# Optimization experiments

Measured on AMD Instinct MI355X. Metric: run time of the kernel, lower is better.

Reference implementation:

```python
import jax, jax.numpy as jnp
import numpy as np

B, C, H, W = 8, 256, 64, 64
RED = 16

def setup_inputs() -> dict:
    key = jax.random.key(0)
    ks = jax.random.split(key, 10)
    s = 0.05
    return {
        "x": jax.random.normal(ks[0], (B, C, H, W), jnp.float32),
        "ca_w1": jax.random.normal(ks[1], (C // RED, C), jnp.float32) * s,
        "ca_w2": jax.random.normal(ks[2], (C, C // RED), jnp.float32) * s,
        "q_w": jax.random.normal(ks[3], (C // RED, C), jnp.float32) * s,
        "q_b": jax.random.normal(ks[4], (C // RED,), jnp.float32) * s,
        "k_w": jax.random.normal(ks[5], (C // RED, C), jnp.float32) * s,
        "k_b": jax.random.normal(ks[6], (C // RED,), jnp.float32) * s,
        "v_w": jax.random.normal(ks[7], (C, C), jnp.float32) * s,
        "v_b": jax.random.normal(ks[8], (C,), jnp.float32) * s,
        "gamma": jax.random.normal(ks[9], (1,), jnp.float32) * s,
    }

def _cbam(x, ca_w1, ca_w2, q_w, q_b, k_w, k_b, v_w, v_b, gamma):
    # ---- Channel attention (squeeze-excite with avg+max pooling) ----
    avg = jnp.mean(x, axis=(2, 3))          # [B, C]
    mx = jnp.max(x, axis=(2, 3))            # [B, C]
    def fc(s):
        h = jax.nn.relu(jnp.einsum('rc,bc->br', ca_w1, s))
        return jnp.einsum('cr,br->bc', ca_w2, h)
    gate = jax.nn.sigmoid(fc(avg) + fc(mx))[:, :, None, None]
    x = x * gate
    # ---- Spatial (non-local) attention ----
    b, c, h, w = x.shape
    hw = h * w
    xf = x.reshape(b, c, hw)                          # [B, C, HW]
    q = jnp.einsum('rc,bcn->brn', q_w, xf) + q_b[None, :, None]   # [B, C/r, HW]
    k = jnp.einsum('rc,bcn->brn', k_w, xf) + k_b[None, :, None]
    v = jnp.einsum('oc,bcn->bon', v_w, xf) + v_b[None, :, None]   # [B, C, HW]
    attn = jax.nn.softmax(jnp.einsum('bri,brj->bij', q, k), axis=-1)  # [B, HW, HW]
    out = jnp.einsum('bcj,bij->bci', v, attn).reshape(b, c, h, w)
    return gamma[0] * out + x

def reference(x, ca_w1, ca_w2, q_w, q_b, k_w, k_b, v_w, v_b, gamma):
    return _cbam(x, ca_w1, ca_w2, q_w, q_b, k_w, k_b, v_w, v_b, gamma)
```

## Files before the change

kernel.cpp:

```cpp
#include <hip/hip_runtime.h>
#include <hip/hip_bf16.h>
#include <math.h>

#define BB 8
#define CCH 256
#define HWN 4096
#define RR 16
#define PSTR 72

typedef __attribute__((ext_vector_type(8))) short short8;
typedef __attribute__((ext_vector_type(4))) float f32x4;

static __device__ __forceinline__ unsigned short f2bf(float x) {
    union { float f; unsigned u; } v; v.f = x;
    return (unsigned short)((v.u + 0x8000u) >> 16);
}
static __device__ __forceinline__ unsigned bfr(float x) {
    union { float f; unsigned u; } v; v.f = x;
    return v.u + 0x8000u;
}

__global__ __launch_bounds__(256) void k_pool(const float* __restrict__ x,
                                              float* __restrict__ avgp,
                                              float* __restrict__ maxp) {
    int bc = blockIdx.x;
    const float4* p = (const float4*)(x + (size_t)bc * HWN);
    int t = threadIdx.x;
    float s = 0.f, m = -INFINITY;
#pragma unroll
    for (int i = 0; i < 4; ++i) {
        float4 v = p[t + 256 * i];
        s += v.x + v.y + v.z + v.w;
        m = fmaxf(m, fmaxf(fmaxf(v.x, v.y), fmaxf(v.z, v.w)));
    }
    for (int off = 32; off; off >>= 1) {
        s += __shfl_down(s, off);
        m = fmaxf(m, __shfl_down(m, off));
    }
    __shared__ float ss[4], sm[4];
    int wid = t >> 6;
    if ((t & 63) == 0) { ss[wid] = s; sm[wid] = m; }
    __syncthreads();
    if (t == 0) {
        float S = ss[0] + ss[1] + ss[2] + ss[3];
        float M = fmaxf(fmaxf(sm[0], sm[1]), fmaxf(sm[2], sm[3]));
        avgp[bc] = S * (1.f / (float)HWN);
        maxp[bc] = M;
    }
}

__global__ __launch_bounds__(256) void k_gate(const float* __restrict__ avgp,
                                              const float* __restrict__ maxp,
                                              const float* __restrict__ w1,
                                              const float* __restrict__ w2,
                                              float* __restrict__ gate) {
    int b = blockIdx.x, t = threadIdx.x;
    __shared__ float sa[CCH], sx[CCH], sh[32];
    sa[t] = avgp[b * CCH + t];
    sx[t] = maxp[b * CCH + t];
    __syncthreads();
    if (t < 32) {
        int r = t & 15;
        const float* src = (t < 16) ? sa : sx;
        float h = 0.f;
        for (int c = 0; c < CCH; ++c) h += w1[r * CCH + c] * src[c];
        sh[t] = fmaxf(h, 0.f);
    }
    __syncthreads();
    float g = 0.f;
#pragma unroll
    for (int r = 0; r < RR; ++r) g += w2[t * RR + r] * (sh[r] + sh[16 + r]);
    gate[b * CCH + t] = 1.f / (1.f + __expf(-g));
}

__global__ __launch_bounds__(256) void k_wprep(const float* __restrict__ vw,
                                               const float* __restrict__ qw,
                                               const float* __restrict__ kw,
                                               unsigned short* __restrict__ Wb) {
    int idx = blockIdx.x * 256 + threadIdx.x;
    int m = idx >> 8, c = idx & 255;
    float v;
    if (m < 256) v = vw[idx];
    else if (m < 272) v = qw[(m - 256) * 256 + c];
    else v = kw[(m - 272) * 256 + c];
    Wb[idx] = f2bf(v);
}

__global__ __launch_bounds__(256) void k_proj(const float* __restrict__ x,
                                              const float* __restrict__ gate,
                                              const unsigned short* __restrict__ Wb,
                                              const float* __restrict__ vb,
                                              const float* __restrict__ qb,
                                              const float* __restrict__ kb,
                                              unsigned short* __restrict__ qT,
                                              unsigned short* __restrict__ kT,
                                              unsigned short* __restrict__ vB) {
    int b = blockIdx.x & 7;
    int n0 = (blockIdx.x >> 3) << 6;
    int t = threadIdx.x;
    int w = t >> 6, l = t & 63, quad = l >> 4, ln = l & 15;

    __shared__ __align__(16) unsigned short xs_t[64][72];
    __shared__ __align__(16) unsigned short vtile[256 * 72];
    __shared__ float qk_s[32][66];

    const f32x4 zf = {0.f, 0.f, 0.f, 0.f};
    f32x4 acc[18];
#pragma unroll
    for (int mt = 0; mt < 18; ++mt) acc[mt] = zf;

    for (int cc = 0; cc < 4; ++cc) {
        __syncthreads();
#pragma unroll
        for (int it = 0; it < 4; ++it) {
            int idx = it * 256 + t;
            int cl = idx >> 4, nq = idx & 15;
            int c = cc * 64 + cl;
            float g = gate[b * CCH + c];
            float4 v = *(const float4*)(x + (((size_t)(b * CCH + c)) << 12) + n0 + nq * 4);
            xs_t[nq * 4 + 0][cl] = f2bf(v.x * g);
            xs_t[nq * 4 + 1][cl] = f2bf(v.y * g);
            xs_t[nq * 4 + 2][cl] = f2bf(v.z * g);
            xs_t[nq * 4 + 3][cl] = f2bf(v.w * g);
        }
        __syncthreads();

        short8 bfrag[2];
#pragma unroll
        for (int kc = 0; kc < 2; ++kc)
            bfrag[kc] = *(const short8*)&xs_t[w * 16 + ln][kc * 32 + quad * 8];

#pragma unroll
        for (int mt = 0; mt < 18; ++mt) {
#pragma unroll
            for (int kc = 0; kc < 2; ++kc) {
                short8 af = *(const short8*)(Wb + ((size_t)(mt * 16 + ln)) * 256 + cc * 64 + kc * 32 + quad * 8);
                acc[mt] = __builtin_amdgcn_mfma_f32_16x16x32_bf16(af, bfrag[kc], acc[mt], 0, 0, 0);
            }
        }
    }

#pragma unroll
    for (int mt = 0; mt < 16; ++mt) {
#pragma unroll
        for (int r = 0; r < 4; ++r) {
            int m = mt * 16 + quad * 4 + r;
            vtile[m * 72 + w * 16 + ln] = f2bf(acc[mt][r] + vb[m]);
        }
    }
#pragma unroll
    for (int r = 0; r < 4; ++r) {
        qk_s[quad * 4 + r][w * 16 + ln] = acc[16][r];
        qk_s[16 + quad * 4 + r][w * 16 + ln] = acc[17][r];
    }
    __syncthreads();

    {
        unsigned short* vBp = vB + (((size_t)b) << 20);
        int c = t;
#pragma unroll
        for (int Q = 0; Q < 8; ++Q) {
            short8 v8 = *(const short8*)(vtile + c * 72 + Q * 8);
            *(short8*)(vBp + ((size_t)((((n0 >> 3) + Q) << 8) + c) << 3)) = v8;
        }
    }
    if (t < 128) {
        int isK = t >> 6;
        int n = t & 63;
        const float* bias = isK ? kb : qb;
        unsigned u32[8];
#pragma unroll
        for (int j = 0; j < 8; ++j) {
            unsigned lo = f2bf(qk_s[isK * 16 + 2 * j][n] + bias[2 * j]);
            unsigned hi = f2bf(qk_s[isK * 16 + 2 * j + 1][n] + bias[2 * j + 1]);
            u32[j] = lo | (hi << 16);
        }
        unsigned short* dst = (isK ? kT : qT) + ((size_t)(b * HWN + n0 + n)) * RR;
        uint4 d0 = {u32[0], u32[1], u32[2], u32[3]};
        uint4 d1 = {u32[4], u32[5], u32[6], u32[7]};
        ((uint4*)dst)[0] = d0;
        ((uint4*)dst)[1] = d1;
    }
}

__global__ __launch_bounds__(512, 4) void k_attn(const unsigned short* __restrict__ qT,
                                                 const unsigned short* __restrict__ kT,
                                                 const unsigned short* __restrict__ vB,
                                                 const float* __restrict__ x,
                                                 const float* __restrict__ gate,
                                                 const float* __restrict__ gamma,
                                                 float* __restrict__ out) {
    int b = blockIdx.x & 7;
    int i0 = (blockIdx.x >> 3) << 5;
    int t = threadIdx.x;
    int w = t >> 6, l = t & 63;
    int quad = l >> 4, ln = l & 15;
    int isub = w & 1, jsub = w >> 1;
    int c0 = w * 32;

    __shared__ __align__(16) unsigned short p_lds[2][32 * PSTR];
    __shared__ float l_s[4][36];

    const short8 zs = {0, 0, 0, 0, 0, 0, 0, 0};
    const f32x4 zf = {0.f, 0.f, 0.f, 0.f};

    short8 bq = zs;
    if (quad < 2)
        bq = *(const short8*)(qT + (((size_t)(b * HWN + i0 + isub * 16 + ln)) << 4) + (quad << 3));

    f32x4 acc[2][2];
#pragma unroll
    for (int cs = 0; cs < 2; ++cs)
#pragma unroll
        for (int is = 0; is < 2; ++is) acc[cs][is] = zf;
    float lsum = 0.f;

    const float c1 = 1.44269504f;
    const float c0e = -11.5415603f;

    const unsigned short* vbase = vB + (((size_t)b) << 20) + ((size_t)c0 << 3);
    const unsigned short* kbase = kT + ((size_t)(b * HWN)) * RR;

    short8 akA = zs, akB = zs;
    short8 avA[4], avB[4];

    auto load_ak = [&](short8& ak, int j0) {
        if (quad < 2)
            ak = *(const short8*)(kbase + (((size_t)(j0 + jsub * 16 + ln)) << 4) + (quad << 3));
    };
    auto load_av = [&](short8 (&av)[4], int j0) {
#pragma unroll
        for (int ks = 0; ks < 2; ++ks)
#pragma unroll
            for (int cs = 0; cs < 2; ++cs) {
                int jc = (j0 >> 3) + ks * 4 + quad;
                av[ks * 2 + cs] = *(const short8*)(vbase + ((size_t)(((jc << 8) + cs * 16 + ln)) << 3));
            }
    };

    load_ak(akA, 0);
    load_av(avA, 0);

    auto step = [&](short8& akC, short8 (&avC)[4], short8& akN, short8 (&avN)[4],
                    unsigned short* pbuf, int j0n, bool pf) {
        f32x4 sf = __builtin_amdgcn_mfma_f32_16x16x32_bf16(akC, bq, zf, 0, 0, 0);

        float p0 = exp2f(fmaf(sf[0], c1, c0e));
        float p1 = exp2f(fmaf(sf[1], c1, c0e));
        float p2 = exp2f(fmaf(sf[2], c1, c0e));
        float p3 = exp2f(fmaf(sf[3], c1, c0e));
        lsum += (p0 + p1) + (p2 + p3);
        uint2 pk;
        pk.x = (bfr(p0) >> 16) | (bfr(p1) & 0xFFFF0000u);
        pk.y = (bfr(p2) >> 16) | (bfr(p3) & 0xFFFF0000u);
        *(uint2*)(pbuf + (isub * 16 + ln) * PSTR + jsub * 16 + quad * 4) = pk;

        __syncthreads();

        if (pf) { load_ak(akN, j0n); load_av(avN, j0n); }

#pragma unroll
        for (int ks = 0; ks < 2; ++ks) {
            short8 bp[2];
#pragma unroll
            for (int is = 0; is < 2; ++is)
                bp[is] = *(const short8*)(pbuf + (is * 16 + ln) * PSTR + ks * 32 + quad * 8);
#pragma unroll
            for (int cs = 0; cs < 2; ++cs)
#pragma unroll
                for (int is = 0; is < 2; ++is)
                    acc[cs][is] = __builtin_amdgcn_mfma_f32_16x16x32_bf16(avC[ks * 2 + cs], bp[is], acc[cs][is], 0, 0, 0);
        }
    };

    for (int jt2 = 0; jt2 < 32; ++jt2) {
        int j0 = jt2 << 7;
        step(akA, avA, akB, avB, &p_lds[0][0], j0 + 64, true);
        step(akB, avB, akA, avA, &p_lds[1][0], (jt2 < 31) ? (j0 + 128) : 0, jt2 < 31);
    }

    lsum += __shfl_xor(lsum, 16, 64);
    lsum += __shfl_xor(lsum, 32, 64);
    if (l < 16) l_s[jsub][isub * 16 + l] = lsum;
    __syncthreads();

    float g = gamma[0];
    float rinv[2];
#pragma unroll
    for (int is = 0; is < 2; ++is) {
        int i = is * 16 + ln;
        float lf = (l_s[0][i] + l_s[1][i]) + (l_s[2][i] + l_s[3][i]);
        rinv[is] = g / lf;
    }

#pragma unroll
    for (int cs = 0; cs < 2; ++cs) {
#pragma unroll
        for (int r = 0; r < 4; ++r) {
            int c = c0 + cs * 16 + quad * 4 + r;
            float gc = gate[b * CCH + c];
            size_t rowoff = (((size_t)(b * CCH + c)) << 12) + i0;
            float* po = out + rowoff;
            const float* px = x + rowoff;
#pragma unroll
            for (int is = 0; is < 2; ++is) {
                int idx = is * 16 + ln;
                po[idx] = acc[cs][is][r] * rinv[is] + px[idx] * gc;
            }
        }
    }
}

extern "C" void kernel_launch(void* const* d_in, const int* in_sizes, int n_in,
                              void* d_out, int out_size, void* d_ws, size_t ws_size,
                              hipStream_t stream) {
    const float* x = (const float*)d_in[0];
    const float* w1 = (const float*)d_in[1];
    const float* w2 = (const float*)d_in[2];
    const float* qw = (const float*)d_in[3];
    const float* qb = (const float*)d_in[4];
    const float* kw = (const float*)d_in[5];
    const float* kb = (const float*)d_in[6];
    const float* vw = (const float*)d_in[7];
    const float* vb = (const float*)d_in[8];
    const float* gamma = (const float*)d_in[9];
    float* out = (float*)d_out;
    char* ws = (char*)d_ws;

    float* avgp = (float*)(ws);
    float* maxp = (float*)(ws + 8192);
    float* gate = (float*)(ws + 16384);
    unsigned short* Wb = (unsigned short*)(ws + 24576);
    unsigned short* qT = (unsigned short*)(ws + 24576 + 147456);
    unsigned short* kT = (unsigned short*)(ws + 24576 + 147456 + 1048576);
    unsigned short* vB = (unsigned short*)(ws + 24576 + 147456 + 2097152);

    k_pool<<<2048, 256, 0, stream>>>(x, avgp, maxp);
    k_wprep<<<288, 256, 0, stream>>>(vw, qw, kw, Wb);
    k_gate<<<8, 256, 0, stream>>>(avgp, maxp, w1, w2, gate);
    k_proj<<<512, 256, 0, stream>>>(x, gate, Wb, vb, qb, kb, qT, kT, vB);
    k_attn<<<1024, 512, 0, stream>>>(qT, kT, vB, x, gate, gamma, out);
}
```

Measured before the change: 257.7 us.

## Restructure attention kernel to 16-query tiles with 4 waves and swizzled LDS

The attention kernel now handles 16 query rows per block with 256 threads (4 waves), launching 2048 blocks instead of 1024. Each wave owns 64 output channels and one 16-key slice of the score tile. The padded P buffer is replaced by an XOR-swizzled 16x64 LDS layout to avoid bank conflicts. The V loads are now issued after the PV MMAs into a single register set rather than double-buffered. Total V and K reads from memory double because each block covers half as many queries. The intent is more resident blocks and fewer registers per thread, but the V prefetch now sits right behind its use, which may expose load latency.

```diff
diff --git a/kernel.cpp b/kernel.cpp
--- a/kernel.cpp
+++ b/kernel.cpp
@@ -6,7 +6,6 @@
 #define CCH 256
 #define HWN 4096
 #define RR 16
-#define PSTR 72
 
 typedef __attribute__((ext_vector_type(8))) short short8;
 typedef __attribute__((ext_vector_type(4))) float f32x4;
@@ -183,7 +182,7 @@
     }
 }
 
-__global__ __launch_bounds__(512, 4) void k_attn(const unsigned short* __restrict__ qT,
+__global__ __launch_bounds__(256, 6) void k_attn(const unsigned short* __restrict__ qT,
                                                  const unsigned short* __restrict__ kT,
                                                  const unsigned short* __restrict__ vB,
                                                  const float* __restrict__ x,
@@ -191,28 +190,25 @@
                                                  const float* __restrict__ gamma,
                                                  float* __restrict__ out) {
     int b = blockIdx.x & 7;
-    int i0 = (blockIdx.x >> 3) << 5;
+    int i0 = (blockIdx.x >> 3) << 4;
     int t = threadIdx.x;
     int w = t >> 6, l = t & 63;
     int quad = l >> 4, ln = l & 15;
-    int isub = w & 1, jsub = w >> 1;
-    int c0 = w * 32;
-
-    __shared__ __align__(16) unsigned short p_lds[2][32 * PSTR];
-    __shared__ float l_s[4][36];
+    int c0 = w * 64;
+
+    __shared__ __align__(16) unsigned short p_lds[2][16 * 64];
+    __shared__ float l_s[4][20];
 
     const short8 zs = {0, 0, 0, 0, 0, 0, 0, 0};
     const f32x4 zf = {0.f, 0.f, 0.f, 0.f};
 
     short8 bq = zs;
     if (quad < 2)
-        bq = *(const short8*)(qT + (((size_t)(b * HWN + i0 + isub * 16 + ln)) << 4) + (quad << 3));
-
-    f32x4 acc[2][2];
-#pragma unroll
-    for (int cs = 0; cs < 2; ++cs)
-#pragma unroll
-        for (int is = 0; is < 2; ++is) acc[cs][is] = zf;
+        bq = *(const short8*)(qT + (((size_t)(b * HWN + i0 + ln)) << 4) + (quad << 3));
+
+    f32x4 acc[4];
+#pragma unroll
+    for (int cs = 0; cs < 4; ++cs) acc[cs] = zf;
     float lsum = 0.f;
 
     const float c1 = 1.44269504f;
@@ -221,30 +217,29 @@
     const unsigned short* vbase = vB + (((size_t)b) << 20) + ((size_t)c0 << 3);
     const unsigned short* kbase = kT + ((size_t)(b * HWN)) * RR;
 
+    int key = ln & 7;
+    int soff = ln * 64 + (((w * 2 + (quad >> 1)) ^ key) * 2 + (quad & 1)) * 4;
+    int roff0 = ln * 64 + ((quad ^ key) << 3);
+    int roff1 = ln * 64 + (((4 + quad) ^ key) << 3);
+
     short8 akA = zs, akB = zs;
-    short8 avA[4], avB[4];
+    short8 av[8];
 
     auto load_ak = [&](short8& ak, int j0) {
         if (quad < 2)
-            ak = *(const short8*)(kbase + (((size_t)(j0 + jsub * 16 + ln)) << 4) + (quad << 3));
+            ak = *(const short8*)(kbase + (((size_t)(j0 + w * 16 + ln)) << 4) + (quad << 3));
     };
-    auto load_av = [&](short8 (&av)[4], int j0) {
+    auto load_av = [&](int j0) {
 #pragma unroll
         for (int ks = 0; ks < 2; ++ks)
 #pragma unroll
-            for (int cs = 0; cs < 2; ++cs) {
+            for (int cs = 0; cs < 4; ++cs) {
                 int jc = (j0 >> 3) + ks * 4 + quad;
-                av[ks * 2 + cs] = *(const short8*)(vbase + ((size_t)(((jc << 8) + cs * 16 + ln)) << 3));
+                av[ks * 4 + cs] = *(const short8*)(vbase + ((size_t)(((jc << 8) + cs * 16 + ln)) << 3));
             }
     };
-
-    load_ak(akA, 0);
-    load_av(avA, 0);
-
-    auto step = [&](short8& akC, short8 (&avC)[4], short8& akN, short8 (&avN)[4],
-                    unsigned short* pbuf, int j0n, bool pf) {
+    auto sstep = [&](short8& akC, unsigned short* pbuf) {
         f32x4 sf = __builtin_amdgcn_mfma_f32_16x16x32_bf16(akC, bq, zf, 0, 0, 0);
-
         float p0 = exp2f(fmaf(sf[0], c1, c0e));
         float p1 = exp2f(fmaf(sf[1], c1, c0e));
         float p2 = exp2f(fmaf(sf[2], c1, c0e));
@@ -253,60 +248,55 @@
         uint2 pk;
         pk.x = (bfr(p0) >> 16) | (bfr(p1) & 0xFFFF0000u);
         pk.y = (bfr(p2) >> 16) | (bfr(p3) & 0xFFFF0000u);
-        *(uint2*)(pbuf + (isub * 16 + ln) * PSTR + jsub * 16 + quad * 4) = pk;
-
-        __syncthreads();
-
-        if (pf) { load_ak(akN, j0n); load_av(avN, j0n); }
-
-#pragma unroll
-        for (int ks = 0; ks < 2; ++ks) {
-            short8 bp[2];
-#pragma unroll
-            for (int is = 0; is < 2; ++is)
-                bp[is] = *(const short8*)(pbuf + (is * 16 + ln) * PSTR + ks * 32 + quad * 8);
-#pragma unroll
-            for (int cs = 0; cs < 2; ++cs)
-#pragma unroll
-                for (int is = 0; is < 2; ++is)
-                    acc[cs][is] = __builtin_amdgcn_mfma_f32_16x16x32_bf16(avC[ks * 2 + cs], bp[is], acc[cs][is], 0, 0, 0);
-        }
+        *(uint2*)(pbuf + soff) = pk;
     };
+    auto pvstep = [&](const unsigned short* pbuf) {
+        short8 bp0 = *(const short8*)(pbuf + roff0);
+#pragma unroll
+        for (int cs = 0; cs < 4; ++cs)
+            acc[cs] = __builtin_amdgcn_mfma_f32_16x16x32_bf16(av[cs], bp0, acc[cs], 0, 0, 0);
+        short8 bp1 = *(const short8*)(pbuf + roff1);
+#pragma unroll
+        for (int cs = 0; cs < 4; ++cs)
+            acc[cs] = __builtin_amdgcn_mfma_f32_16x16x32_bf16(av[4 + cs], bp1, acc[cs], 0, 0, 0);
+    };
+
+    load_ak(akA, 0);
+    load_av(0);
 
     for (int jt2 = 0; jt2 < 32; ++jt2) {
         int j0 = jt2 << 7;
-        step(akA, avA, akB, avB, &p_lds[0][0], j0 + 64, true);
-        step(akB, avB, akA, avA, &p_lds[1][0], (jt2 < 31) ? (j0 + 128) : 0, jt2 < 31);
+        sstep(akA, &p_lds[0][0]);
+        __syncthreads();
+        load_ak(akB, j0 + 64);
+        pvstep(&p_lds[0][0]);
+        load_av(j0 + 64);
+
+        int j0n = (jt2 < 31) ? (j0 + 128) : 0;
+        sstep(akB, &p_lds[1][0]);
+        __syncthreads();
+        load_ak(akA, j0n);
+        pvstep(&p_lds[1][0]);
+        load_av(j0n);
     }
 
     lsum += __shfl_xor(lsum, 16, 64);
     lsum += __shfl_xor(lsum, 32, 64);
-    if (l < 16) l_s[jsub][isub * 16 + l] = lsum;
+    if (l < 16) l_s[w][l] = lsum;
     __syncthreads();
 
     float g = gamma[0];
-    float rinv[2];
-#pragma unroll
-    for (int is = 0; is < 2; ++is) {
-        int i = is * 16 + ln;
-        float lf = (l_s[0][i] + l_s[1][i]) + (l_s[2][i] + l_s[3][i]);
-        rinv[is] = g / lf;
-    }
-
-#pragma unroll
-    for (int cs = 0; cs < 2; ++cs) {
+    float lf = (l_s[0][ln] + l_s[1][ln]) + (l_s[2][ln] + l_s[3][ln]);
+    float rinv = g / lf;
+
+#pragma unroll
+    for (int cs = 0; cs < 4; ++cs) {
 #pragma unroll
         for (int r = 0; r < 4; ++r) {
             int c = c0 + cs * 16 + quad * 4 + r;
             float gc = gate[b * CCH + c];
             size_t rowoff = (((size_t)(b * CCH + c)) << 12) + i0;
-            float* po = out + rowoff;
-            const float* px = x + rowoff;
-#pragma unroll
-            for (int is = 0; is < 2; ++is) {
-                int idx = is * 16 + ln;
-                po[idx] = acc[cs][is][r] * rinv[is] + px[idx] * gc;
-            }
+            out[rowoff + ln] = acc[cs][r] * rinv + x[rowoff + ln] * gc;
         }
     }
 }
@@ -339,5 +329,5 @@
     k_wprep<<<288, 256, 0, stream>>>(vw, qw, kw, Wb);
     k_gate<<<8, 256, 0, stream>>>(avgp, maxp, w1, w2, gate);
     k_proj<<<512, 256, 0, stream>>>(x, gate, Wb, vb, qb, kb, qT, kT, vB);
-    k_attn<<<1024, 512, 0, stream>>>(qT, kT, vB, x, gate, gamma, out);
-}
+    k_attn<<<2048, 256, 0, stream>>>(qT, kT, vB, x, gate, gamma, out);
+}
```

Result: slower. 557.3 us (+116.2%).

## Double attention query tile to 64 rows to halve V streaming per block

Applied to the files above, without the earlier changes.

Each attention block now covers 64 query positions instead of 32, with the 8 waves split 4 along i and 2 along j. Every V and K tile loaded is therefore reused for twice as many query rows, roughly halving V and K traffic across the grid, and each wave issues more MFMAs per softmax tile. The V prefetch is now single-buffered and issued after the PV MFMAs, and the LDS row stride changes from 72 to 68. The cost is fewer blocks (512), more accumulator registers, and less load-latency hiding for V.

```diff
diff --git a/kernel.cpp b/kernel.cpp
--- a/kernel.cpp
+++ b/kernel.cpp
@@ -6,7 +6,7 @@
 #define CCH 256
 #define HWN 4096
 #define RR 16
-#define PSTR 72
+#define PSTR 68
 
 typedef __attribute__((ext_vector_type(8))) short short8;
 typedef __attribute__((ext_vector_type(4))) float f32x4;
@@ -191,28 +191,28 @@
                                                  const float* __restrict__ gamma,
                                                  float* __restrict__ out) {
     int b = blockIdx.x & 7;
-    int i0 = (blockIdx.x >> 3) << 5;
+    int i0 = (blockIdx.x >> 3) << 6;
     int t = threadIdx.x;
     int w = t >> 6, l = t & 63;
     int quad = l >> 4, ln = l & 15;
-    int isub = w & 1, jsub = w >> 1;
+    int iw = w & 3, jw = w >> 2;
     int c0 = w * 32;
 
-    __shared__ __align__(16) unsigned short p_lds[2][32 * PSTR];
-    __shared__ float l_s[4][36];
+    __shared__ __align__(16) unsigned short p_lds[2][64 * PSTR];
+    __shared__ float l_s[8][20];
 
     const short8 zs = {0, 0, 0, 0, 0, 0, 0, 0};
     const f32x4 zf = {0.f, 0.f, 0.f, 0.f};
 
     short8 bq = zs;
     if (quad < 2)
-        bq = *(const short8*)(qT + (((size_t)(b * HWN + i0 + isub * 16 + ln)) << 4) + (quad << 3));
-
-    f32x4 acc[2][2];
+        bq = *(const short8*)(qT + (((size_t)(b * HWN + i0 + iw * 16 + ln)) << 4) + (quad << 3));
+
+    f32x4 acc[2][4];
 #pragma unroll
     for (int cs = 0; cs < 2; ++cs)
 #pragma unroll
-        for (int is = 0; is < 2; ++is) acc[cs][is] = zf;
+        for (int is = 0; is < 4; ++is) acc[cs][is] = zf;
     float lsum = 0.f;
 
     const float c1 = 1.44269504f;
@@ -221,14 +221,22 @@
     const unsigned short* vbase = vB + (((size_t)b) << 20) + ((size_t)c0 << 3);
     const unsigned short* kbase = kT + ((size_t)(b * HWN)) * RR;
 
-    short8 akA = zs, akB = zs;
-    short8 avA[4], avB[4];
-
-    auto load_ak = [&](short8& ak, int j0) {
-        if (quad < 2)
-            ak = *(const short8*)(kbase + (((size_t)(j0 + jsub * 16 + ln)) << 4) + (quad << 3));
+    int soff0 = (iw * 16 + ln) * PSTR + jw * 32 + quad * 4;
+    int soff1 = soff0 + 16;
+
+    short8 akA[2], akB[2];
+    short8 av[4];
+#pragma unroll
+    for (int jt = 0; jt < 2; ++jt) { akA[jt] = zs; akB[jt] = zs; }
+
+    auto load_ak = [&](short8 (&ak)[2], int j0) {
+        if (quad < 2) {
+#pragma unroll
+            for (int jt = 0; jt < 2; ++jt)
+                ak[jt] = *(const short8*)(kbase + (((size_t)(j0 + jw * 32 + jt * 16 + ln)) << 4) + (quad << 3));
+        }
     };
-    auto load_av = [&](short8 (&av)[4], int j0) {
+    auto load_av = [&](int j0) {
 #pragma unroll
         for (int ks = 0; ks < 2; ++ks)
 #pragma unroll
@@ -237,61 +245,71 @@
                 av[ks * 2 + cs] = *(const short8*)(vbase + ((size_t)(((jc << 8) + cs * 16 + ln)) << 3));
             }
     };
-
-    load_ak(akA, 0);
-    load_av(avA, 0);
-
-    auto step = [&](short8& akC, short8 (&avC)[4], short8& akN, short8 (&avN)[4],
-                    unsigned short* pbuf, int j0n, bool pf) {
-        f32x4 sf = __builtin_amdgcn_mfma_f32_16x16x32_bf16(akC, bq, zf, 0, 0, 0);
-
-        float p0 = exp2f(fmaf(sf[0], c1, c0e));
-        float p1 = exp2f(fmaf(sf[1], c1, c0e));
-        float p2 = exp2f(fmaf(sf[2], c1, c0e));
-        float p3 = exp2f(fmaf(sf[3], c1, c0e));
-        lsum += (p0 + p1) + (p2 + p3);
+    auto sstep = [&](short8 (&akC)[2], unsigned short* pbuf) {
+        f32x4 sf0 = __builtin_amdgcn_mfma_f32_16x16x32_bf16(akC[0], bq, zf, 0, 0, 0);
+        f32x4 sf1 = __builtin_amdgcn_mfma_f32_16x16x32_bf16(akC[1], bq, zf, 0, 0, 0);
+        float p0 = exp2f(fmaf(sf0[0], c1, c0e));
+        float p1 = exp2f(fmaf(sf0[1], c1, c0e));
+        float p2 = exp2f(fmaf(sf0[2], c1, c0e));
+        float p3 = exp2f(fmaf(sf0[3], c1, c0e));
+        float q0 = exp2f(fmaf(sf1[0], c1, c0e));
+        float q1 = exp2f(fmaf(sf1[1], c1, c0e));
+        float q2 = exp2f(fmaf(sf1[2], c1, c0e));
+        float q3 = exp2f(fmaf(sf1[3], c1, c0e));
+        lsum += ((p0 + p1) + (p2 + p3)) + ((q0 + q1) + (q2 + q3));
         uint2 pk;
         pk.x = (bfr(p0) >> 16) | (bfr(p1) & 0xFFFF0000u);
         pk.y = (bfr(p2) >> 16) | (bfr(p3) & 0xFFFF0000u);
-        *(uint2*)(pbuf + (isub * 16 + ln) * PSTR + jsub * 16 + quad * 4) = pk;
-
-        __syncthreads();
-
-        if (pf) { load_ak(akN, j0n); load_av(avN, j0n); }
-
+        *(uint2*)(pbuf + soff0) = pk;
+        uint2 qk;
+        qk.x = (bfr(q0) >> 16) | (bfr(q1) & 0xFFFF0000u);
+        qk.y = (bfr(q2) >> 16) | (bfr(q3) & 0xFFFF0000u);
+        *(uint2*)(pbuf + soff1) = qk;
+    };
+    auto pvstep = [&](const unsigned short* pbuf) {
 #pragma unroll
         for (int ks = 0; ks < 2; ++ks) {
-            short8 bp[2];
-#pragma unroll
-            for (int is = 0; is < 2; ++is)
+            short8 bp[4];
+#pragma unroll
+            for (int is = 0; is < 4; ++is)
                 bp[is] = *(const short8*)(pbuf + (is * 16 + ln) * PSTR + ks * 32 + quad * 8);
 #pragma unroll
             for (int cs = 0; cs < 2; ++cs)
 #pragma unroll
-                for (int is = 0; is < 2; ++is)
-                    acc[cs][is] = __builtin_amdgcn_mfma_f32_16x16x32_bf16(avC[ks * 2 + cs], bp[is], acc[cs][is], 0, 0, 0);
+                for (int is = 0; is < 4; ++is)
+                    acc[cs][is] = __builtin_amdgcn_mfma_f32_16x16x32_bf16(av[ks * 2 + cs], bp[is], acc[cs][is], 0, 0, 0);
         }
     };
+
+    load_ak(akA, 0);
+    load_av(0);
 
     for (int jt2 = 0; jt2 < 32; ++jt2) {
         int j0 = jt2 << 7;
-        step(akA, avA, akB, avB, &p_lds[0][0], j0 + 64, true);
-        step(akB, avB, akA, avA, &p_lds[1][0], (jt2 < 31) ? (j0 + 128) : 0, jt2 < 31);
+        sstep(akA, &p_lds[0][0]);
+        __syncthreads();
+        load_ak(akB, j0 + 64);
+        pvstep(&p_lds[0][0]);
+        load_av(j0 + 64);
+
+        int j0n = (jt2 < 31) ? (j0 + 128) : 0;
+        sstep(akB, &p_lds[1][0]);
+        __syncthreads();
+        load_ak(akA, j0n);
+        pvstep(&p_lds[1][0]);
+        load_av(j0n);
     }
 
     lsum += __shfl_xor(lsum, 16, 64);
     lsum += __shfl_xor(lsum, 32, 64);
-    if (l < 16) l_s[jsub][isub * 16 + l] = lsum;
+    if (l < 16) l_s[w][l] = lsum;
     __syncthreads();
 
     float g = gamma[0];
-    float rinv[2];
-#pragma unroll
-    for (int is = 0; is < 2; ++is) {
-        int i = is * 16 + ln;
-        float lf = (l_s[0][i] + l_s[1][i]) + (l_s[2][i] + l_s[3][i]);
-        rinv[is] = g / lf;
-    }
+    float rinv[4];
+#pragma unroll
+    for (int is = 0; is < 4; ++is)
+        rinv[is] = g / (l_s[is][ln] + l_s[is + 4][ln]);
 
 #pragma unroll
     for (int cs = 0; cs < 2; ++cs) {
@@ -303,7 +321,7 @@
             float* po = out + rowoff;
             const float* px = x + rowoff;
 #pragma unroll
-            for (int is = 0; is < 2; ++is) {
+            for (int is = 0; is < 4; ++is) {
                 int idx = is * 16 + ln;
                 po[idx] = acc[cs][is][r] * rinv[is] + px[idx] * gc;
             }
@@ -339,5 +357,5 @@
     k_wprep<<<288, 256, 0, stream>>>(vw, qw, kw, Wb);
     k_gate<<<8, 256, 0, stream>>>(avgp, maxp, w1, w2, gate);
     k_proj<<<512, 256, 0, stream>>>(x, gate, Wb, vb, qb, kb, qT, kT, vB);
-    k_attn<<<1024, 512, 0, stream>>>(qT, kT, vB, x, gate, gamma, out);
-}
+    k_attn<<<512, 512, 0, stream>>>(qT, kT, vB, x, gate, gamma, out);
+}
```

Measured after the change: 403.5 us. 1.57x slower.
